# Performance work log

Measured on AMD Instinct MI355X. Metric: run time of the kernel, lower is better.

The kernel has to match this reference:

```python
import jax, jax.numpy as jnp
import numpy as np

RADIUS = 0.2
NSAMPLE = 32
BANDWIDTH = 0.1


def ellipsoid_query(xyz, new_xyz, radius, nsample):
    """xyz:(B,N,3), new_xyz:(B,P,3) -> idx:(B,P,nsample) int32.
    Ellipsoid semi-axes (radius, 2*radius, radius); first nsample hits,
    padded with the first hit (index 0 if empty), matching the CUDA kernel.
    """
    B, N, _ = xyz.shape
    inv_sq = jnp.asarray([1.0 / radius**2, 1.0 / (2.0 * radius) ** 2, 1.0 / radius**2],
                         dtype=xyz.dtype)
    # accumulate per-coordinate to avoid a (B,P,N,3) intermediate
    q = jnp.zeros((B, new_xyz.shape[1], N), dtype=xyz.dtype)
    for k in range(3):
        d = new_xyz[:, :, None, k] - xyz[:, None, :, k]  # (B,P,N)
        q = q + d * d * inv_sq[k]
    mask = q < 1.0
    cand = jnp.where(mask, jnp.arange(N, dtype=jnp.int32), jnp.int32(N))  # invalid -> N
    cand = jnp.sort(cand, axis=-1)[..., :nsample]                          # (B,P,S)
    first = cand[..., :1]
    first = jnp.where(first >= N, jnp.int32(0), first)
    return jnp.where(cand >= N, first, cand)


def group(features, idx):
    """features:(B,C,N), idx:(B,P,S) -> (B,C,P,S)"""
    return jnp.take_along_axis(features[:, :, None, :], idx[:, None, :, :], axis=-1)


def setup_inputs() -> dict:
    key = jax.random.key(0)
    k1, k2, k3 = jax.random.split(key, 3)
    xyz = jax.random.uniform(k1, (4, 8192, 3), dtype=jnp.float32)
    new_xyz = jax.random.uniform(k2, (4, 2048, 3), dtype=jnp.float32)
    features = jax.random.normal(k3, (4, 64, 8192), dtype=jnp.float32)
    return {"xyz": xyz, "new_xyz": new_xyz, "features": features}


def reference(xyz, new_xyz, features):
    idx = ellipsoid_query(xyz, new_xyz, RADIUS, NSAMPLE)          # (B,P,S)
    xyz_trans = jnp.transpose(xyz, (0, 2, 1))                      # (B,3,N)
    grouped_xyz = group(xyz_trans, idx)                            # (B,3,P,S)
    # density: gaussian of distance to center
    g = jnp.transpose(grouped_xyz, (0, 2, 3, 1))                   # (B,P,S,3)
    dist = jnp.linalg.norm(g - new_xyz[:, :, None, :], axis=-1)    # (B,P,S)
    density = jnp.exp(-dist**2 / (2.0 * BANDWIDTH**2)) / (2.5 * BANDWIDTH)
    grouped_density = (1.0 / density)[:, None, :, :]               # (B,1,P,S)
    grouped_features = group(features, idx)                        # (B,C,P,S)
    return jnp.concatenate([grouped_xyz, grouped_density, grouped_features], axis=1)
```

## Files before the change

kernel.cpp:

```cpp
#include <hip/hip_runtime.h>

constexpr int NPTS = 8192;
constexpr int NQ   = 2048;
constexpr int NC   = 64;
constexpr int NS   = 32;
constexpr int QPB  = 8;
constexpr int NCH  = 3 + 1 + NC;
constexpr int CS   = NQ * NS;

__global__ __launch_bounds__(256, 8) void transpose_feat_kernel(
    const float* __restrict__ feat,
    float* __restrict__ ftr)
{
    __shared__ float tile[NC][65];

    const int b  = blockIdx.y;
    const int n0 = blockIdx.x * 64;
    const int t  = threadIdx.x;

    const float* fb = feat + (size_t)b * NC * NPTS;
    {
        const int pl = t & 63;
        const int c0 = t >> 6;
        #pragma unroll
        for (int i = 0; i < 16; ++i) {
            const int c = c0 + 4 * i;
            tile[c][pl] = fb[(size_t)c * NPTS + n0 + pl];
        }
    }
    __syncthreads();
    float* tb = ftr + ((size_t)b * NPTS + n0) * NC;
    {
        const int cl = t & 63;
        const int pb = t >> 6;
        #pragma unroll
        for (int i = 0; i < 16; ++i) {
            const int pp = pb + 4 * i;
            tb[(size_t)pp * NC + cl] = tile[cl][pp];
        }
    }
}

__device__ __forceinline__ void ellipsoid_scan(
    const float* __restrict__ xb, const float* __restrict__ nxyz,
    int b, int p, int lane, int* __restrict__ idx_row)
{
    const float qx = nxyz[((size_t)b * NQ + p) * 3 + 0];
    const float qy = nxyz[((size_t)b * NQ + p) * 3 + 1];
    const float qz = nxyz[((size_t)b * NQ + p) * 3 + 2];

    int cnt = 0;
    int first = -1;

    for (int base = 0; base < NPTS; base += 64) {
        const int i = base + lane;
        const float x = xb[i * 3 + 0];
        const float y = xb[i * 3 + 1];
        const float z = xb[i * 3 + 2];
        const float dx = __fsub_rn(qx, x);
        const float dy = __fsub_rn(qy, y);
        const float dz = __fsub_rn(qz, z);
        const float t0 = __fmul_rn(__fmul_rn(dx, dx), 25.0f);
        const float t1 = __fmul_rn(__fmul_rn(dy, dy), 6.25f);
        const float t2 = __fmul_rn(__fmul_rn(dz, dz), 25.0f);
        const float qv = __fadd_rn(__fadd_rn(t0, t1), t2);
        const bool hit = qv < 1.0f;

        const unsigned long long m = __ballot(hit);
        if (first < 0 && m != 0ull)
            first = base + __builtin_ctzll(m);
        if (hit) {
            const int pos = cnt + __popcll(m & ((1ull << lane) - 1ull));
            if (pos < NS) idx_row[pos] = i;
        }
        cnt += __popcll(m);
        if (cnt >= NS) break;
    }
    if (cnt < NS) {
        const int f = (cnt == 0) ? 0 : first;
        if (lane < NS && lane >= cnt) idx_row[lane] = f;
    }
}

__device__ __forceinline__ void write_xyz_density(
    const float* __restrict__ xb, const float* __restrict__ nxyz,
    int b, int p, int j, float* __restrict__ ob)
{
    const float qx = nxyz[((size_t)b * NQ + p) * 3 + 0];
    const float qy = nxyz[((size_t)b * NQ + p) * 3 + 1];
    const float qz = nxyz[((size_t)b * NQ + p) * 3 + 2];
    const float px = xb[j * 3 + 0];
    const float py = xb[j * 3 + 1];
    const float pz = xb[j * 3 + 2];

    const float dx = __fsub_rn(px, qx);
    const float dy = __fsub_rn(py, qy);
    const float dz = __fsub_rn(pz, qz);
    const float d2 = __fadd_rn(__fadd_rn(__fmul_rn(dx, dx), __fmul_rn(dy, dy)),
                               __fmul_rn(dz, dz));
    const float dist = __fsqrt_rn(d2);
    const float arg  = __fdiv_rn(-__fmul_rn(dist, dist), 0.02f);
    const float density = __fmul_rn(expf(arg), 4.0f);
    const float gd = __fdiv_rn(1.0f, density);

    ob[0 * (size_t)CS] = px;
    ob[1 * (size_t)CS] = py;
    ob[2 * (size_t)CS] = pz;
    ob[3 * (size_t)CS] = gd;
}

__global__ __launch_bounds__(512, 8) void ellip_main_t_kernel(
    const float* __restrict__ xyz,
    const float* __restrict__ nxyz,
    const float* __restrict__ ftr,
    float* __restrict__ out)
{
    __shared__ int idx_s[QPB][NS];

    const int b    = blockIdx.y;
    const int p0   = blockIdx.x * QPB;
    const int tid  = threadIdx.x;
    const int lane = tid & 63;
    const int wave = tid >> 6;

    const float* xb = xyz + (size_t)b * NPTS * 3;

    ellipsoid_scan(xb, nxyz, b, p0 + wave, lane, idx_s[wave]);
    __syncthreads();

    const int q = tid >> 6;
    const int r = tid & 63;
    const int p = p0 + q;
    const int s = r & 31;
    const int j = idx_s[q][s];

    float* ob = out + ((size_t)b * NCH * NQ + p) * NS + s;

    if (r < 32)
        write_xyz_density(xb, nxyz, b, p, j, ob);

    const float4* fp = (const float4*)(ftr + ((size_t)b * NPTS + j) * NC);
    const int cg0 = r >> 5;
    #pragma unroll
    for (int k = 0; k < 8; ++k) {
        const int cg = cg0 + 2 * k;
        const float4 v = fp[cg];
        float* oc = ob + (size_t)(4 + 4 * cg) * CS;
        oc[0 * (size_t)CS] = v.x;
        oc[1 * (size_t)CS] = v.y;
        oc[2 * (size_t)CS] = v.z;
        oc[3 * (size_t)CS] = v.w;
    }
}

__global__ __launch_bounds__(512, 8) void ellip_main_direct_kernel(
    const float* __restrict__ xyz,
    const float* __restrict__ nxyz,
    const float* __restrict__ feat,
    float* __restrict__ out)
{
    __shared__ int idx_s[QPB][NS];

    const int b    = blockIdx.y;
    const int p0   = blockIdx.x * QPB;
    const int tid  = threadIdx.x;
    const int lane = tid & 63;
    const int wave = tid >> 6;

    const float* xb = xyz + (size_t)b * NPTS * 3;

    ellipsoid_scan(xb, nxyz, b, p0 + wave, lane, idx_s[wave]);
    __syncthreads();

    const int s = tid & 31;
    const int h = (tid >> 5) & 1;
    const int q = tid >> 6;
    const int p = p0 + q;
    const int j = idx_s[q][s];

    float* ob = out + ((size_t)b * NCH * NQ + p) * NS + s;

    if (h == 0)
        write_xyz_density(xb, nxyz, b, p, j, ob);

    const float* fb = feat + (size_t)b * NC * NPTS + j;
    #pragma unroll 4
    for (int c = h; c < NC; c += 2)
        ob[(size_t)(4 + c) * CS] = fb[(size_t)c * NPTS];
}

extern "C" void kernel_launch(void* const* d_in, const int* in_sizes, int n_in,
                              void* d_out, int out_size, void* d_ws, size_t ws_size,
                              hipStream_t stream) {
    const float* xyz  = (const float*)d_in[0];
    const float* nxyz = (const float*)d_in[1];
    const float* feat = (const float*)d_in[2];
    float* out = (float*)d_out;

    const int B = in_sizes[0] / (NPTS * 3);
    const size_t trans_bytes = (size_t)B * NPTS * NC * sizeof(float);

    if (ws_size >= trans_bytes) {
        float* ftr = (float*)d_ws;
        transpose_feat_kernel<<<dim3(NPTS / 64, B), 256, 0, stream>>>(feat, ftr);
        ellip_main_t_kernel<<<dim3(NQ / QPB, B), 512, 0, stream>>>(xyz, nxyz, ftr, out);
    } else {
        ellip_main_direct_kernel<<<dim3(NQ / QPB, B), 512, 0, stream>>>(xyz, nxyz, feat, out);
    }
}
```

Measured before the change: 113.3 us.

## Split scan and gather into separate kernels with SoA xyz and prefetching

Adds an SoA conversion of xyz to the prep kernel. The ellipsoid scan moves into its own 256-thread kernel that keeps coalesced SoA loads two iterations ahead in registers, then writes the xyz/density channels and stores the indices to workspace. A separate group kernel gathers the transposed features using those indices. The goal is to stop slow scanning waves from stalling the gather inside one block and to make the scan loads coalesced, at the cost of an extra launch and a round trip of the indices through global memory.

```diff
diff --git a/kernel.cpp b/kernel.cpp
--- a/kernel.cpp
+++ b/kernel.cpp
@@ -4,47 +4,79 @@
 constexpr int NQ   = 2048;
 constexpr int NC   = 64;
 constexpr int NS   = 32;
-constexpr int QPB  = 8;
 constexpr int NCH  = 3 + 1 + NC;
 constexpr int CS   = NQ * NS;
 
-__global__ __launch_bounds__(256, 8) void transpose_feat_kernel(
+
+__global__ __launch_bounds__(256, 8) void prep_kernel(
     const float* __restrict__ feat,
-    float* __restrict__ ftr)
-{
-    __shared__ float tile[NC][65];
-
+    const float* __restrict__ xyz,
+    float* __restrict__ ftr,
+    float* __restrict__ soa)
+{
     const int b  = blockIdx.y;
-    const int n0 = blockIdx.x * 64;
+    const int bx = blockIdx.x;
     const int t  = threadIdx.x;
 
-    const float* fb = feat + (size_t)b * NC * NPTS;
-    {
-        const int pl = t & 63;
-        const int c0 = t >> 6;
+    if (bx < NPTS / 64) {
+        __shared__ float tile[NC][65];
+        const int n0 = bx * 64;
+        const float* fb = feat + (size_t)b * NC * NPTS;
+        {
+            const int pl = t & 63;
+            const int c0 = t >> 6;
+            #pragma unroll
+            for (int i = 0; i < 16; ++i) {
+                const int c = c0 + 4 * i;
+                tile[c][pl] = fb[(size_t)c * NPTS + n0 + pl];
+            }
+        }
+        __syncthreads();
+        float* tb = ftr + ((size_t)b * NPTS + n0) * NC;
+        {
+            const int cl = t & 63;
+            const int pb = t >> 6;
+            #pragma unroll
+            for (int i = 0; i < 16; ++i) {
+                const int pp = pb + 4 * i;
+                tb[(size_t)pp * NC + cl] = tile[cl][pp];
+            }
+        }
+    } else {
+        const int n0 = (bx - NPTS / 64) * 4096;
+        const float* xb = xyz + (size_t)b * NPTS * 3;
+        float* xs = soa + (size_t)b * 3 * NPTS;
+        float* ys = xs + NPTS;
+        float* zs = ys + NPTS;
         #pragma unroll
-        for (int i = 0; i < 16; ++i) {
-            const int c = c0 + 4 * i;
-            tile[c][pl] = fb[(size_t)c * NPTS + n0 + pl];
-        }
-    }
-    __syncthreads();
-    float* tb = ftr + ((size_t)b * NPTS + n0) * NC;
-    {
-        const int cl = t & 63;
-        const int pb = t >> 6;
-        #pragma unroll
-        for (int i = 0; i < 16; ++i) {
-            const int pp = pb + 4 * i;
-            tb[(size_t)pp * NC + cl] = tile[cl][pp];
-        }
-    }
-}
-
-__device__ __forceinline__ void ellipsoid_scan(
-    const float* __restrict__ xb, const float* __restrict__ nxyz,
-    int b, int p, int lane, int* __restrict__ idx_row)
-{
+        for (int k = 0; k < 16; ++k) {
+            const int i = n0 + k * 256 + t;
+            xs[i] = xb[i * 3 + 0];
+            ys[i] = xb[i * 3 + 1];
+            zs[i] = xb[i * 3 + 2];
+        }
+    }
+}
+
+__global__ __launch_bounds__(256, 8) void scan_kernel(
+    const float* __restrict__ soa,
+    const float* __restrict__ nxyz,
+    int* __restrict__ gidx,
+    float* __restrict__ out)
+{
+    __shared__ int idx_s[4][NS];
+
+    const int b    = blockIdx.y;
+    const int tid  = threadIdx.x;
+    const int lane = tid & 63;
+    const int wave = tid >> 6;
+    const int p    = blockIdx.x * 4 + wave;
+
+    const float* xs = soa + (size_t)b * 3 * NPTS;
+    const float* ys = xs + NPTS;
+    const float* zs = ys + NPTS;
+    int* idx_row = idx_s[wave];
+
     const float qx = nxyz[((size_t)b * NQ + p) * 3 + 0];
     const float qy = nxyz[((size_t)b * NQ + p) * 3 + 1];
     const float qz = nxyz[((size_t)b * NQ + p) * 3 + 2];
@@ -52,14 +84,19 @@
     int cnt = 0;
     int first = -1;
 
+    float x0 = xs[lane],      y0 = ys[lane],      z0 = zs[lane];
+    float x1 = xs[64 + lane], y1 = ys[64 + lane], z1 = zs[64 + lane];
+
     for (int base = 0; base < NPTS; base += 64) {
-        const int i = base + lane;
-        const float x = xb[i * 3 + 0];
-        const float y = xb[i * 3 + 1];
-        const float z = xb[i * 3 + 2];
-        const float dx = __fsub_rn(qx, x);
-        const float dy = __fsub_rn(qy, y);
-        const float dz = __fsub_rn(qz, z);
+        float xn = 0.f, yn = 0.f, zn = 0.f;
+        const int pf = base + 128;
+        if (pf < NPTS) {
+            xn = xs[pf + lane]; yn = ys[pf + lane]; zn = zs[pf + lane];
+        }
+
+        const float dx = __fsub_rn(qx, x0);
+        const float dy = __fsub_rn(qy, y0);
+        const float dz = __fsub_rn(qz, z0);
         const float t0 = __fmul_rn(__fmul_rn(dx, dx), 25.0f);
         const float t1 = __fmul_rn(__fmul_rn(dy, dy), 6.25f);
         const float t2 = __fmul_rn(__fmul_rn(dz, dz), 25.0f);
@@ -71,74 +108,58 @@
             first = base + __builtin_ctzll(m);
         if (hit) {
             const int pos = cnt + __popcll(m & ((1ull << lane) - 1ull));
-            if (pos < NS) idx_row[pos] = i;
+            if (pos < NS) idx_row[pos] = base + lane;
         }
         cnt += __popcll(m);
         if (cnt >= NS) break;
+
+        x0 = x1; y0 = y1; z0 = z1;
+        x1 = xn; y1 = yn; z1 = zn;
     }
     if (cnt < NS) {
         const int f = (cnt == 0) ? 0 : first;
         if (lane < NS && lane >= cnt) idx_row[lane] = f;
     }
-}
-
-__device__ __forceinline__ void write_xyz_density(
-    const float* __restrict__ xb, const float* __restrict__ nxyz,
-    int b, int p, int j, float* __restrict__ ob)
-{
-    const float qx = nxyz[((size_t)b * NQ + p) * 3 + 0];
-    const float qy = nxyz[((size_t)b * NQ + p) * 3 + 1];
-    const float qz = nxyz[((size_t)b * NQ + p) * 3 + 2];
-    const float px = xb[j * 3 + 0];
-    const float py = xb[j * 3 + 1];
-    const float pz = xb[j * 3 + 2];
-
-    const float dx = __fsub_rn(px, qx);
-    const float dy = __fsub_rn(py, qy);
-    const float dz = __fsub_rn(pz, qz);
-    const float d2 = __fadd_rn(__fadd_rn(__fmul_rn(dx, dx), __fmul_rn(dy, dy)),
-                               __fmul_rn(dz, dz));
-    const float dist = __fsqrt_rn(d2);
-    const float arg  = __fdiv_rn(-__fmul_rn(dist, dist), 0.02f);
-    const float density = __fmul_rn(expf(arg), 4.0f);
-    const float gd = __fdiv_rn(1.0f, density);
-
-    ob[0 * (size_t)CS] = px;
-    ob[1 * (size_t)CS] = py;
-    ob[2 * (size_t)CS] = pz;
-    ob[3 * (size_t)CS] = gd;
-}
-
-__global__ __launch_bounds__(512, 8) void ellip_main_t_kernel(
-    const float* __restrict__ xyz,
-    const float* __restrict__ nxyz,
+
+    if (lane < NS) {
+        const int s = lane;
+        const int j = idx_row[s];
+        gidx[((size_t)b * NQ + p) * NS + s] = j;
+
+        const float px = xs[j], py = ys[j], pz = zs[j];
+        const float dx = __fsub_rn(px, qx);
+        const float dy = __fsub_rn(py, qy);
+        const float dz = __fsub_rn(pz, qz);
+        const float d2 = __fadd_rn(__fadd_rn(__fmul_rn(dx, dx), __fmul_rn(dy, dy)),
+                                   __fmul_rn(dz, dz));
+        const float dist = __fsqrt_rn(d2);
+        const float arg  = __fdiv_rn(-__fmul_rn(dist, dist), 0.02f);
+        const float density = __fmul_rn(expf(arg), 4.0f);
+        const float gd = __fdiv_rn(1.0f, density);
+
+        float* ob = out + ((size_t)b * NCH * NQ + p) * NS + s;
+        ob[0 * (size_t)CS] = px;
+        ob[1 * (size_t)CS] = py;
+        ob[2 * (size_t)CS] = pz;
+        ob[3 * (size_t)CS] = gd;
+    }
+}
+
+__global__ __launch_bounds__(512, 8) void group_kernel(
+    const int* __restrict__ gidx,
     const float* __restrict__ ftr,
     float* __restrict__ out)
 {
-    __shared__ int idx_s[QPB][NS];
-
-    const int b    = blockIdx.y;
-    const int p0   = blockIdx.x * QPB;
-    const int tid  = threadIdx.x;
-    const int lane = tid & 63;
-    const int wave = tid >> 6;
-
-    const float* xb = xyz + (size_t)b * NPTS * 3;
-
-    ellipsoid_scan(xb, nxyz, b, p0 + wave, lane, idx_s[wave]);
-    __syncthreads();
-
-    const int q = tid >> 6;
-    const int r = tid & 63;
-    const int p = p0 + q;
-    const int s = r & 31;
-    const int j = idx_s[q][s];
+    const int b   = blockIdx.y;
+    const int tid = threadIdx.x;
+    const int q   = tid >> 6;
+    const int r   = tid & 63;
+    const int s   = r & 31;
+    const int p   = blockIdx.x * 8 + q;
+
+    const int j = gidx[((size_t)b * NQ + p) * NS + s];
 
     float* ob = out + ((size_t)b * NCH * NQ + p) * NS + s;
-
-    if (r < 32)
-        write_xyz_density(xb, nxyz, b, p, j, ob);
-
     const float4* fp = (const float4*)(ftr + ((size_t)b * NPTS + j) * NC);
     const int cg0 = r >> 5;
     #pragma unroll
@@ -153,23 +174,51 @@
     }
 }
 
-__global__ __launch_bounds__(512, 8) void ellip_main_direct_kernel(
+__global__ __launch_bounds__(512, 8) void ellip_direct_kernel(
     const float* __restrict__ xyz,
     const float* __restrict__ nxyz,
     const float* __restrict__ feat,
     float* __restrict__ out)
 {
-    __shared__ int idx_s[QPB][NS];
+    __shared__ int idx_s[8][NS];
 
     const int b    = blockIdx.y;
-    const int p0   = blockIdx.x * QPB;
+    const int p0   = blockIdx.x * 8;
     const int tid  = threadIdx.x;
     const int lane = tid & 63;
     const int wave = tid >> 6;
-
     const float* xb = xyz + (size_t)b * NPTS * 3;
 
-    ellipsoid_scan(xb, nxyz, b, p0 + wave, lane, idx_s[wave]);
+    {
+        const int p = p0 + wave;
+        const float qx = nxyz[((size_t)b * NQ + p) * 3 + 0];
+        const float qy = nxyz[((size_t)b * NQ + p) * 3 + 1];
+        const float qz = nxyz[((size_t)b * NQ + p) * 3 + 2];
+        int cnt = 0, first = -1;
+        for (int base = 0; base < NPTS; base += 64) {
+            const int i = base + lane;
+            const float dx = __fsub_rn(qx, xb[i * 3 + 0]);
+            const float dy = __fsub_rn(qy, xb[i * 3 + 1]);
+            const float dz = __fsub_rn(qz, xb[i * 3 + 2]);
+            const float t0 = __fmul_rn(__fmul_rn(dx, dx), 25.0f);
+            const float t1 = __fmul_rn(__fmul_rn(dy, dy), 6.25f);
+            const float t2 = __fmul_rn(__fmul_rn(dz, dz), 25.0f);
+            const float qv = __fadd_rn(__fadd_rn(t0, t1), t2);
+            const bool hit = qv < 1.0f;
+            const unsigned long long m = __ballot(hit);
+            if (first < 0 && m != 0ull) first = base + __builtin_ctzll(m);
+            if (hit) {
+                const int pos = cnt + __popcll(m & ((1ull << lane) - 1ull));
+                if (pos < NS) idx_s[wave][pos] = i;
+            }
+            cnt += __popcll(m);
+            if (cnt >= NS) break;
+        }
+        if (cnt < NS) {
+            const int f = (cnt == 0) ? 0 : first;
+            if (lane < NS && lane >= cnt) idx_s[wave][lane] = f;
+        }
+    }
     __syncthreads();
 
     const int s = tid & 31;
@@ -177,12 +226,26 @@
     const int q = tid >> 6;
     const int p = p0 + q;
     const int j = idx_s[q][s];
-
     float* ob = out + ((size_t)b * NCH * NQ + p) * NS + s;
 
-    if (h == 0)
-        write_xyz_density(xb, nxyz, b, p, j, ob);
-
+    if (h == 0) {
+        const float qx = nxyz[((size_t)b * NQ + p) * 3 + 0];
+        const float qy = nxyz[((size_t)b * NQ + p) * 3 + 1];
+        const float qz = nxyz[((size_t)b * NQ + p) * 3 + 2];
+        const float px = xb[j * 3 + 0], py = xb[j * 3 + 1], pz = xb[j * 3 + 2];
+        const float dx = __fsub_rn(px, qx);
+        const float dy = __fsub_rn(py, qy);
+        const float dz = __fsub_rn(pz, qz);
+        const float d2 = __fadd_rn(__fadd_rn(__fmul_rn(dx, dx), __fmul_rn(dy, dy)),
+                                   __fmul_rn(dz, dz));
+        const float dist = __fsqrt_rn(d2);
+        const float arg  = __fdiv_rn(-__fmul_rn(dist, dist), 0.02f);
+        const float gd = __fdiv_rn(1.0f, __fmul_rn(expf(arg), 4.0f));
+        ob[0 * (size_t)CS] = px;
+        ob[1 * (size_t)CS] = py;
+        ob[2 * (size_t)CS] = pz;
+        ob[3 * (size_t)CS] = gd;
+    }
     const float* fb = feat + (size_t)b * NC * NPTS + j;
     #pragma unroll 4
     for (int c = h; c < NC; c += 2)
@@ -198,13 +261,20 @@
     float* out = (float*)d_out;
 
     const int B = in_sizes[0] / (NPTS * 3);
-    const size_t trans_bytes = (size_t)B * NPTS * NC * sizeof(float);
-
-    if (ws_size >= trans_bytes) {
+    const size_t ftr_f = (size_t)B * NPTS * NC;
+    const size_t soa_f = (size_t)B * 3 * NPTS;
+    const size_t idx_f = (size_t)B * NQ * NS;
+    const size_t need  = (ftr_f + soa_f + idx_f) * 4;
+
+    if (ws_size >= need) {
         float* ftr = (float*)d_ws;
-        transpose_feat_kernel<<<dim3(NPTS / 64, B), 256, 0, stream>>>(feat, ftr);
-        ellip_main_t_kernel<<<dim3(NQ / QPB, B), 512, 0, stream>>>(xyz, nxyz, ftr, out);
+        float* soa = ftr + ftr_f;
+        int*   idx = (int*)(soa + soa_f);
+
+        prep_kernel<<<dim3(NPTS / 64 + 2, B), 256, 0, stream>>>(feat, xyz, ftr, soa);
+        scan_kernel<<<dim3(NQ / 4, B), 256, 0, stream>>>(soa, nxyz, idx, out);
+        group_kernel<<<dim3(NQ / 8, B), 512, 0, stream>>>(idx, ftr, out);
     } else {
-        ellip_main_direct_kernel<<<dim3(NQ / QPB, B), 512, 0, stream>>>(xyz, nxyz, feat, out);
-    }
-}
+        ellip_direct_kernel<<<dim3(NQ / 8, B), 512, 0, stream>>>(xyz, nxyz, feat, out);
+    }
+}
```

Measured after the change: 113.4 us. About the same (+0.0%).
